# Optimization experiments

Hardware: AMD Instinct MI355X
Metric: run time of the kernel (lower is better)

The kernel has to match this reference:

```python
import jax, jax.numpy as jnp
import numpy as np

NUM_CLASSES = 81
B, P = 32, 32768

def setup_inputs() -> dict:
    key = jax.random.key(0)
    k1, k2, k3, k4, k5 = jax.random.split(key, 5)
    loc_t = jax.random.normal(k1, (B, P, 4), jnp.float32)
    loc_data = jax.random.normal(k2, (B, P, 4), jnp.float32)
    conf_data = jax.random.normal(k3, (B, P, NUM_CLASSES), jnp.float32)
    r = jax.random.uniform(k4, (B, P))
    cls = jax.random.randint(k5, (B, P), 1, NUM_CLASSES)
    conf_t = jnp.where(r < 0.02, cls, jnp.where(r < 0.04, -1, 0)).astype(jnp.int32)
    return {"loc_t": loc_t, "loc_data": loc_data, "conf_t": conf_t, "conf_data": conf_data}

def reference(loc_t, loc_data, conf_t, conf_data):
    num, num_priors, C = conf_data.shape
    pos = conf_t > 0           # [B,P] positive anchors
    regard = conf_t == -1      # [B,P] ignored anchors
    conf_t = jnp.where(regard, 0, conf_t)

    # ---- localization: smooth L1 over positive anchors, summed ----
    diff = jnp.abs(loc_data - loc_t)
    sl1 = jnp.where(diff < 1.0, 0.5 * diff * diff, diff - 0.5)
    loss_l = jnp.sum(sl1 * pos[..., None].astype(sl1.dtype))

    # ---- hard-negative mining score (log_sum_exp with GLOBAL max, as in source) ----
    m = jax.lax.stop_gradient(jnp.max(conf_data))
    lse_global = jnp.log(jnp.sum(jnp.exp(conf_data - m), axis=-1)) + m  # [B,P]
    gathered = jnp.take_along_axis(conf_data, conf_t[..., None], axis=-1)[..., 0]  # [B,P]
    loss_c = lse_global - gathered
    loss_c = jnp.where(pos | regard, 0.0, loss_c)

    # double argsort -> rank of each anchor in descending loss order
    order = jnp.argsort(-loss_c, axis=1)
    rank = jnp.argsort(order, axis=1)
    num_pos = jnp.sum(pos, axis=1, keepdims=True)                     # [B,1]
    num_neg = jnp.minimum(3 * num_pos, num_priors - 1)                # [B,1]
    neg = rank < num_neg                                              # [B,P]

    # ---- classification: cross-entropy over pos|neg anchors, summed ----
    ce = jax.nn.logsumexp(conf_data, axis=-1) - gathered              # [B,P]
    loss_conf = jnp.sum(jnp.where(pos | neg, ce, 0.0))

    N = jnp.sum(num_pos).astype(jnp.float32)
    return (loss_l / N, loss_conf / N)
```

## Files before the change

### kernel.cpp

```cpp
#include <hip/hip_runtime.h>
#include <cstdint>

#define NUM_CLASSES 81
#define BB 32
#define PP 32768
#define CA 64
#define TPB 256
#define CHUNK_FLOATS (CA * NUM_CLASSES)
#define CHUNK_F4 (CHUNK_FLOATS / 4)
#define NCHUNK (BB * PP / CA)
#define GRID_MAIN 768
#define NP_STRIDE 32

__device__ __forceinline__ unsigned f2key(float f) {
    unsigned u = __float_as_uint(f);
    return u ^ (unsigned)(((int)u >> 31) | (int)0x80000000u);
}
__device__ __forceinline__ float key2f(unsigned k) {
    unsigned u = (k & 0x80000000u) ? (k ^ 0x80000000u) : ~k;
    return __uint_as_float(u);
}


__global__ void mbl_zero_kernel(unsigned* __restrict__ p, int n) {
    int i = blockIdx.x * 256 + threadIdx.x;
    if (i < n) p[i] = 0u;
}

__global__ __launch_bounds__(TPB, 4) void mbl_main_kernel(
    const float* __restrict__ loc_t, const float* __restrict__ loc_data,
    const int* __restrict__ conf_t, const float* __restrict__ conf,
    float* __restrict__ loss_c, float* __restrict__ acc, int* __restrict__ num_pos)
{
    __shared__ __align__(16) float tile[2][CHUNK_FLOATS];
    __shared__ float wred[2][TPB / 64];

    const int t = threadIdx.x;
    const int lane = t & 63;
    const int w = t >> 6;
    const int q = lane >> 4;
    const int a_loc = (w << 4) | (lane & 15);

    float sum_ll = 0.f, sum_pce = 0.f;

    int c = blockIdx.x;
    {
        const float4* src = (const float4*)(conf + (size_t)c * CHUNK_FLOATS);
        float4* dst = (float4*)tile[0];
        #pragma unroll
        for (int i = 0; i < 5; ++i) dst[t + i * TPB] = src[t + i * TPB];
        if (t < CHUNK_F4 - 5 * TPB) dst[t + 5 * TPB] = src[t + 5 * TPB];
    }
    int parity = 0;
    const int stride = gridDim.x;
    for (; c < NCHUNK; c += stride) {
        __syncthreads();
        const int nc = c + stride;
        if (nc < NCHUNK) {
            const float4* src = (const float4*)(conf + (size_t)nc * CHUNK_FLOATS);
            float4* dst = (float4*)tile[parity ^ 1];
            #pragma unroll
            for (int i = 0; i < 5; ++i) dst[t + i * TPB] = src[t + i * TPB];
            if (t < CHUNK_F4 - 5 * TPB) dst[t + 5 * TPB] = src[t + 5 * TPB];
        }
        const float* cp = tile[parity] + a_loc * NUM_CLASSES + q * 20;
        float s = 0.f;
        #pragma unroll
        for (int j = 0; j < 20; ++j) s += __expf(cp[j]);
        if (q == 3) s += __expf(cp[20]);
        s += __shfl_xor(s, 16);
        s += __shfl_xor(s, 32);

        bool posl = false;
        if (q == 0) {
            const int idx = c * CA + a_loc;
            const int label = conf_t[idx];
            posl = label > 0;
            const bool regard = label == -1;
            const int lab = label < 0 ? 0 : label;
            const float g = tile[parity][a_loc * NUM_CLASSES + lab];
            const float ce = __logf(s) - g;
            loss_c[idx] = (posl || regard) ? 0.f : ce;
            if (posl) {
                float4 a4 = ((const float4*)loc_data)[idx];
                float4 b4 = ((const float4*)loc_t)[idx];
                float d0 = fabsf(a4.x - b4.x), d1 = fabsf(a4.y - b4.y);
                float d2 = fabsf(a4.z - b4.z), d3 = fabsf(a4.w - b4.w);
                sum_ll += (d0 < 1.f) ? 0.5f * d0 * d0 : d0 - 0.5f;
                sum_ll += (d1 < 1.f) ? 0.5f * d1 * d1 : d1 - 0.5f;
                sum_ll += (d2 < 1.f) ? 0.5f * d2 * d2 : d2 - 0.5f;
                sum_ll += (d3 < 1.f) ? 0.5f * d3 * d3 : d3 - 0.5f;
                sum_pce += ce;
            }
        }
        unsigned long long bal = __ballot(posl);
        if (lane == 0 && bal)
            atomicAdd(&num_pos[(c >> 9) * NP_STRIDE], (int)__popcll(bal));
        parity ^= 1;
    }
    #pragma unroll
    for (int off = 32; off > 0; off >>= 1) {
        sum_ll += __shfl_down(sum_ll, off);
        sum_pce += __shfl_down(sum_pce, off);
    }
    if (lane == 0) { wred[0][w] = sum_ll; wred[1][w] = sum_pce; }
    __syncthreads();
    if (t == 0) {
        float s0 = 0.f, s1 = 0.f;
        #pragma unroll
        for (int i = 0; i < TPB / 64; ++i) { s0 += wred[0][i]; s1 += wred[1][i]; }
        atomicAdd(&acc[0], s0);
        atomicAdd(&acc[1], s1);
    }
}

__global__ __launch_bounds__(256) void mbl_hist_kernel(
    const float* __restrict__ loss_c, const unsigned* __restrict__ prefix,
    unsigned* __restrict__ ghist, int shift, unsigned mask)
{
    const int b = blockIdx.x >> 4;
    const int slice = blockIdx.x & 15;
    const int t = threadIdx.x;
    __shared__ unsigned h[256];
    h[t] = 0u;
    __syncthreads();
    const unsigned pref = prefix[b];
    const float4* r4 = (const float4*)(loss_c + (size_t)b * PP + slice * 2048);
    #pragma unroll
    for (int i = 0; i < 2; ++i) {
        float4 v = r4[t + 256 * i];
        unsigned k0 = f2key(v.x), k1 = f2key(v.y), k2 = f2key(v.z), k3 = f2key(v.w);
        if ((k0 & mask) == pref) atomicAdd(&h[(k0 >> shift) & 255u], 1u);
        if ((k1 & mask) == pref) atomicAdd(&h[(k1 >> shift) & 255u], 1u);
        if ((k2 & mask) == pref) atomicAdd(&h[(k2 >> shift) & 255u], 1u);
        if ((k3 & mask) == pref) atomicAdd(&h[(k3 >> shift) & 255u], 1u);
    }
    __syncthreads();
    unsigned cnt = h[t];
    if (cnt) atomicAdd(&ghist[b * 256 + t], cnt);
}

__global__ __launch_bounds__(256) void mbl_pick_kernel(
    unsigned* __restrict__ ghist, unsigned* __restrict__ prefix,
    unsigned* __restrict__ remaining, const int* __restrict__ num_pos,
    int shift, int first)
{
    const int b = blockIdx.x;
    const int t = threadIdx.x;
    __shared__ unsigned suf[256];
    __shared__ unsigned sh_k;
    if (t == 0) {
        unsigned k;
        if (first) {
            int kk = 3 * num_pos[b * NP_STRIDE];
            if (kk > PP - 1) kk = PP - 1;
            if (kk <= 0) { prefix[b] = 0xFFFFFFFFu; remaining[b] = 0u; k = 0u; }
            else k = (unsigned)kk;
        } else {
            k = remaining[b];
        }
        sh_k = k;
    }
    __syncthreads();
    const unsigned krem = sh_k;
    if (krem == 0u) return;

    unsigned hv = ghist[b * 256 + t];
    ghist[b * 256 + t] = 0u;
    suf[t] = hv;
    __syncthreads();
    #pragma unroll
    for (int step = 1; step < 256; step <<= 1) {
        unsigned v = suf[t] + ((t + step < 256) ? suf[t + step] : 0u);
        __syncthreads();
        suf[t] = v;
        __syncthreads();
    }
    const unsigned above = (t == 255) ? 0u : suf[t + 1];
    if (suf[t] >= krem && above < krem) {
        prefix[b] |= ((unsigned)t) << shift;
        remaining[b] = krem - above;
    }
}

__global__ __launch_bounds__(256) void mbl_sum_kernel(
    const float* __restrict__ loss_c, const unsigned* __restrict__ prefix,
    float* __restrict__ acc)
{
    const int b = blockIdx.x >> 4;
    const int slice = blockIdx.x & 15;
    const int t = threadIdx.x;
    const int lane = t & 63;
    const int w = t >> 6;
    const unsigned T = prefix[b];
    const float4* r4 = (const float4*)(loss_c + (size_t)b * PP + slice * 2048);
    float partial = 0.f;
    #pragma unroll
    for (int i = 0; i < 2; ++i) {
        float4 v = r4[t + 256 * i];
        if (f2key(v.x) > T) partial += v.x;
        if (f2key(v.y) > T) partial += v.y;
        if (f2key(v.z) > T) partial += v.z;
        if (f2key(v.w) > T) partial += v.w;
    }
    #pragma unroll
    for (int off = 32; off > 0; off >>= 1) partial += __shfl_down(partial, off);
    __shared__ float r[4];
    if (lane == 0) r[w] = partial;
    __syncthreads();
    if (t == 0) atomicAdd(&acc[2], r[0] + r[1] + r[2] + r[3]);
}

__global__ void mbl_final_kernel(const float* __restrict__ acc,
                                 const int* __restrict__ num_pos,
                                 const unsigned* __restrict__ prefix,
                                 const unsigned* __restrict__ remaining,
                                 float* __restrict__ out)
{
    if (threadIdx.x == 0 && blockIdx.x == 0) {
        int n = 0;
        float extra = 0.f;
        for (int i = 0; i < BB; ++i) {
            n += num_pos[i * NP_STRIDE];
            unsigned rem = remaining[i];
            if (rem) extra += (float)rem * key2f(prefix[i]);
        }
        const float N = (float)n;
        out[0] = acc[0] / N;
        out[1] = (acc[1] + acc[2] + extra) / N;
    }
}

extern "C" void kernel_launch(void* const* d_in, const int* in_sizes, int n_in,
                              void* d_out, int out_size, void* d_ws, size_t ws_size,
                              hipStream_t stream) {
    const float* loc_t    = (const float*)d_in[0];
    const float* loc_data = (const float*)d_in[1];
    const int*   conf_t   = (const int*)d_in[2];
    const float* conf     = (const float*)d_in[3];
    float* out = (float*)d_out;

    char* ws = (char*)d_ws;
    const size_t off0 = (size_t)BB * PP * sizeof(float);
    float*    loss_c    = (float*)ws;
    float*    acc       = (float*)(ws + off0);
    int*      num_pos   = (int*)(ws + off0 + 256);
    unsigned* prefix    = (unsigned*)(ws + off0 + 4608);
    unsigned* remaining = (unsigned*)(ws + off0 + 4864);
    unsigned* ghist     = (unsigned*)(ws + off0 + 5120);

    mbl_zero_kernel<<<37, 256, 0, stream>>>((unsigned*)(ws + off0), 9472);

    mbl_main_kernel<<<GRID_MAIN, TPB, 0, stream>>>(
        loc_t, loc_data, conf_t, conf, loss_c, acc, num_pos);

    const unsigned masks[4] = {0x00000000u, 0xFF000000u, 0xFFFF0000u, 0xFFFFFF00u};
    for (int p = 0; p < 4; ++p) {
        const int shift = 24 - 8 * p;
        mbl_hist_kernel<<<512, 256, 0, stream>>>(loss_c, prefix, ghist, shift, masks[p]);
        mbl_pick_kernel<<<BB, 256, 0, stream>>>(ghist, prefix, remaining, num_pos,
                                                shift, p == 0 ? 1 : 0);
    }
    mbl_sum_kernel<<<512, 256, 0, stream>>>(loss_c, prefix, acc);
    mbl_final_kernel<<<1, 64, 0, stream>>>(acc, num_pos, prefix, remaining, out);
}
```

Before: 512.9 us.

## Replace multi-pass radix select with single-block-per-batch histogram select; async LDS loads

The main kernel now uses 32-anchor chunks with 8 threads per anchor, a larger grid and higher occupancy bound. It loads conf tiles with global_load_lds direct-to-LDS copies instead of register round-trips. The four hist/pick launch pairs and the separate sum kernel are replaced by one 1024-thread block per batch. That block builds a 4096-bin count and sum histogram, collects the boundary bin into an LDS list, then refines it with two more histogram levels. This removes about ten kernel launches and repeated passes over loss_c. The cost is only 32 blocks doing serial scans, and the boundary list is capped at 16384 entries.

```diff
diff --git a/kernel.cpp b/kernel.cpp
--- a/kernel.cpp
+++ b/kernel.cpp
@@ -4,13 +4,15 @@
 #define NUM_CLASSES 81
 #define BB 32
 #define PP 32768
-#define CA 64
+#define CA 32
 #define TPB 256
 #define CHUNK_FLOATS (CA * NUM_CLASSES)
 #define CHUNK_F4 (CHUNK_FLOATS / 4)
 #define NCHUNK (BB * PP / CA)
-#define GRID_MAIN 768
+#define GRID_MAIN 1792
 #define NP_STRIDE 32
+#define NBIN 4096
+#define LCAP 16384
 
 __device__ __forceinline__ unsigned f2key(float f) {
     unsigned u = __float_as_uint(f);
@@ -21,13 +23,16 @@
     return __uint_as_float(u);
 }
 
+#define GLDS16(gp, lp) __builtin_amdgcn_global_load_lds( \
+    (const __attribute__((address_space(1))) void*)(gp), \
+    (__attribute__((address_space(3))) void*)(lp), 16, 0, 0)
+
 
 __global__ void mbl_zero_kernel(unsigned* __restrict__ p, int n) {
-    int i = blockIdx.x * 256 + threadIdx.x;
-    if (i < n) p[i] = 0u;
-}
-
-__global__ __launch_bounds__(TPB, 4) void mbl_main_kernel(
+    for (int i = threadIdx.x; i < n; i += 1024) p[i] = 0u;
+}
+
+__global__ __launch_bounds__(TPB, 7) void mbl_main_kernel(
     const float* __restrict__ loc_t, const float* __restrict__ loc_data,
     const int* __restrict__ conf_t, const float* __restrict__ conf,
     float* __restrict__ loss_c, float* __restrict__ acc, int* __restrict__ num_pos)
@@ -37,49 +42,50 @@
 
     const int t = threadIdx.x;
     const int lane = t & 63;
-    const int w = t >> 6;
-    const int q = lane >> 4;
-    const int a_loc = (w << 4) | (lane & 15);
+    const int g = t >> 3;
+    const int r = t & 7;
 
     float sum_ll = 0.f, sum_pce = 0.f;
 
     int c = blockIdx.x;
     {
-        const float4* src = (const float4*)(conf + (size_t)c * CHUNK_FLOATS);
-        float4* dst = (float4*)tile[0];
-        #pragma unroll
-        for (int i = 0; i < 5; ++i) dst[t + i * TPB] = src[t + i * TPB];
-        if (t < CHUNK_F4 - 5 * TPB) dst[t + 5 * TPB] = src[t + 5 * TPB];
-    }
+        const float4* s4 = (const float4*)(conf + (size_t)c * CHUNK_FLOATS);
+        float4* d4 = (float4*)tile[0];
+        GLDS16(s4 + t, d4 + t);
+        GLDS16(s4 + t + 256, d4 + t + 256);
+        if (t < CHUNK_F4 - 512) GLDS16(s4 + t + 512, d4 + t + 512);
+    }
+    __syncthreads();
+
     int parity = 0;
     const int stride = gridDim.x;
     for (; c < NCHUNK; c += stride) {
-        __syncthreads();
         const int nc = c + stride;
         if (nc < NCHUNK) {
-            const float4* src = (const float4*)(conf + (size_t)nc * CHUNK_FLOATS);
-            float4* dst = (float4*)tile[parity ^ 1];
-            #pragma unroll
-            for (int i = 0; i < 5; ++i) dst[t + i * TPB] = src[t + i * TPB];
-            if (t < CHUNK_F4 - 5 * TPB) dst[t + 5 * TPB] = src[t + 5 * TPB];
-        }
-        const float* cp = tile[parity] + a_loc * NUM_CLASSES + q * 20;
+            const float4* s4 = (const float4*)(conf + (size_t)nc * CHUNK_FLOATS);
+            float4* d4 = (float4*)tile[parity ^ 1];
+            GLDS16(s4 + t, d4 + t);
+            GLDS16(s4 + t + 256, d4 + t + 256);
+            if (t < CHUNK_F4 - 512) GLDS16(s4 + t + 512, d4 + t + 512);
+        }
+        const float* cp = tile[parity] + g * NUM_CLASSES + r * 10;
         float s = 0.f;
         #pragma unroll
-        for (int j = 0; j < 20; ++j) s += __expf(cp[j]);
-        if (q == 3) s += __expf(cp[20]);
-        s += __shfl_xor(s, 16);
-        s += __shfl_xor(s, 32);
+        for (int j = 0; j < 10; ++j) s += __expf(cp[j]);
+        if (r == 0) s += __expf(tile[parity][g * NUM_CLASSES + 80]);
+        s += __shfl_xor(s, 1);
+        s += __shfl_xor(s, 2);
+        s += __shfl_xor(s, 4);
 
         bool posl = false;
-        if (q == 0) {
-            const int idx = c * CA + a_loc;
+        if (r == 0) {
+            const int idx = c * CA + g;
             const int label = conf_t[idx];
             posl = label > 0;
             const bool regard = label == -1;
             const int lab = label < 0 ? 0 : label;
-            const float g = tile[parity][a_loc * NUM_CLASSES + lab];
-            const float ce = __logf(s) - g;
+            const float gv = tile[parity][g * NUM_CLASSES + lab];
+            const float ce = __logf(s) - gv;
             loss_c[idx] = (posl || regard) ? 0.f : ce;
             if (posl) {
                 float4 a4 = ((const float4*)loc_data)[idx];
@@ -95,7 +101,8 @@
         }
         unsigned long long bal = __ballot(posl);
         if (lane == 0 && bal)
-            atomicAdd(&num_pos[(c >> 9) * NP_STRIDE], (int)__popcll(bal));
+            atomicAdd(&num_pos[(c >> 10) * NP_STRIDE], (int)__popcll(bal));
+        __syncthreads();
         parity ^= 1;
     }
     #pragma unroll
@@ -103,6 +110,7 @@
         sum_ll += __shfl_down(sum_ll, off);
         sum_pce += __shfl_down(sum_pce, off);
     }
+    const int w = t >> 6;
     if (lane == 0) { wred[0][w] = sum_ll; wred[1][w] = sum_pce; }
     __syncthreads();
     if (t == 0) {
@@ -114,120 +122,154 @@
     }
 }
 
-__global__ __launch_bounds__(256) void mbl_hist_kernel(
-    const float* __restrict__ loss_c, const unsigned* __restrict__ prefix,
-    unsigned* __restrict__ ghist, int shift, unsigned mask)
+__global__ __launch_bounds__(1024) void mbl_select_kernel(
+    const float* __restrict__ loss_c, const int* __restrict__ num_pos,
+    float* __restrict__ acc)
 {
-    const int b = blockIdx.x >> 4;
-    const int slice = blockIdx.x & 15;
-    const int t = threadIdx.x;
-    __shared__ unsigned h[256];
-    h[t] = 0u;
-    __syncthreads();
-    const unsigned pref = prefix[b];
-    const float4* r4 = (const float4*)(loss_c + (size_t)b * PP + slice * 2048);
-    #pragma unroll
-    for (int i = 0; i < 2; ++i) {
-        float4 v = r4[t + 256 * i];
-        unsigned k0 = f2key(v.x), k1 = f2key(v.y), k2 = f2key(v.z), k3 = f2key(v.w);
-        if ((k0 & mask) == pref) atomicAdd(&h[(k0 >> shift) & 255u], 1u);
-        if ((k1 & mask) == pref) atomicAdd(&h[(k1 >> shift) & 255u], 1u);
-        if ((k2 & mask) == pref) atomicAdd(&h[(k2 >> shift) & 255u], 1u);
-        if ((k3 & mask) == pref) atomicAdd(&h[(k3 >> shift) & 255u], 1u);
-    }
-    __syncthreads();
-    unsigned cnt = h[t];
-    if (cnt) atomicAdd(&ghist[b * 256 + t], cnt);
-}
-
-__global__ __launch_bounds__(256) void mbl_pick_kernel(
-    unsigned* __restrict__ ghist, unsigned* __restrict__ prefix,
-    unsigned* __restrict__ remaining, const int* __restrict__ num_pos,
-    int shift, int first)
-{
+    __shared__ unsigned cnt[NBIN];
+    __shared__ float fsum[NBIN];
+    __shared__ float list[LCAP];
+    __shared__ unsigned sh_nlist, sh_B, sh_r, sh_D1, sh_r2, sh_D0, sh_rem;
+    __shared__ float sh_above;
+    __shared__ float wr[16];
+
     const int b = blockIdx.x;
     const int t = threadIdx.x;
-    __shared__ unsigned suf[256];
-    __shared__ unsigned sh_k;
+    int k = 3 * num_pos[b * NP_STRIDE];
+    if (k > PP - 1) k = PP - 1;
+    if (k <= 0) return;
+
+    #pragma unroll
+    for (int i = 0; i < NBIN / 1024; ++i) { cnt[t + i * 1024] = 0u; fsum[t + i * 1024] = 0.f; }
+    if (t == 0) sh_nlist = 0u;
+    __syncthreads();
+
+    const float4* r4 = (const float4*)(loss_c + (size_t)b * PP);
+    float4 vv[8];
+    #pragma unroll
+    for (int i = 0; i < 8; ++i) vv[i] = r4[t + i * 1024];
+    #pragma unroll
+    for (int i = 0; i < 8; ++i) {
+        float vals[4] = {vv[i].x, vv[i].y, vv[i].z, vv[i].w};
+        #pragma unroll
+        for (int j = 0; j < 4; ++j) {
+            float v = vals[j];
+            unsigned bin = (f2key(v) >> 19) - 4096u;
+            bin = bin > 4095u ? 4095u : bin;
+            atomicAdd(&cnt[bin], 1u);
+            atomicAdd(&fsum[bin], v);
+        }
+    }
+    __syncthreads();
+
+    for (int step = 1; step < NBIN; step <<= 1) {
+        unsigned c0[4]; float s0[4];
+        #pragma unroll
+        for (int i = 0; i < 4; ++i) {
+            int j = t + i * 1024, jj = j + step;
+            c0[i] = cnt[j] + (jj < NBIN ? cnt[jj] : 0u);
+            s0[i] = fsum[j] + (jj < NBIN ? fsum[jj] : 0.f);
+        }
+        __syncthreads();
+        #pragma unroll
+        for (int i = 0; i < 4; ++i) { int j = t + i * 1024; cnt[j] = c0[i]; fsum[j] = s0[i]; }
+        __syncthreads();
+    }
+    const unsigned kk = (unsigned)k;
+    #pragma unroll
+    for (int i = 0; i < 4; ++i) {
+        int j = t + i * 1024;
+        unsigned here = cnt[j], above = (j < NBIN - 1) ? cnt[j + 1] : 0u;
+        if (here >= kk && above < kk) {
+            sh_B = (unsigned)j; sh_r = kk - above;
+            sh_above = (j < NBIN - 1) ? fsum[j + 1] : 0.f;
+        }
+    }
+    __syncthreads();
+    const unsigned B = sh_B;
+    const unsigned r = sh_r;
+    const float sum_above = sh_above;
+
+    #pragma unroll
+    for (int i = 0; i < 8; ++i) {
+        float vals[4] = {vv[i].x, vv[i].y, vv[i].z, vv[i].w};
+        #pragma unroll
+        for (int j = 0; j < 4; ++j) {
+            float v = vals[j];
+            unsigned bin = (f2key(v) >> 19) - 4096u;
+            bin = bin > 4095u ? 4095u : bin;
+            if (bin == B) { unsigned p = atomicAdd(&sh_nlist, 1u); if (p < LCAP) list[p] = v; }
+        }
+    }
+    __syncthreads();
+    unsigned n = sh_nlist; if (n > LCAP) n = LCAP;
+
+    cnt[t] = 0u;
+    __syncthreads();
+    for (unsigned e = t; e < n; e += 1024)
+        atomicAdd(&cnt[(f2key(list[e]) >> 9) & 1023u], 1u);
+    __syncthreads();
+    for (int step = 1; step < 1024; step <<= 1) {
+        unsigned v = cnt[t] + (t + step < 1024 ? cnt[t + step] : 0u);
+        __syncthreads(); cnt[t] = v; __syncthreads();
+    }
+    {
+        unsigned here = cnt[t], above = (t < 1023) ? cnt[t + 1] : 0u;
+        if (here >= r && above < r) { sh_D1 = (unsigned)t; sh_r2 = r - above; }
+    }
+    __syncthreads();
+    const unsigned D1 = sh_D1;
+    const unsigned r2 = sh_r2;
+
+    if (t < 512) cnt[t] = 0u;
+    __syncthreads();
+    for (unsigned e = t; e < n; e += 1024) {
+        unsigned key = f2key(list[e]);
+        if (((key >> 9) & 1023u) == D1) atomicAdd(&cnt[key & 511u], 1u);
+    }
+    __syncthreads();
+    for (int step = 1; step < 512; step <<= 1) {
+        unsigned v = 0u;
+        if (t < 512) v = cnt[t] + (t + step < 512 ? cnt[t + step] : 0u);
+        __syncthreads();
+        if (t < 512) cnt[t] = v;
+        __syncthreads();
+    }
+    if (t < 512) {
+        unsigned here = cnt[t], above = (t < 511) ? cnt[t + 1] : 0u;
+        if (here >= r2 && above < r2) { sh_D0 = (unsigned)t; sh_rem = r2 - above; }
+    }
+    __syncthreads();
+    const unsigned T = ((B + 4096u) << 19) | (D1 << 9) | sh_D0;
+    const unsigned rem = sh_rem;
+
+    float part = 0.f;
+    for (unsigned e = t; e < n; e += 1024) {
+        float v = list[e];
+        if (f2key(v) > T) part += v;
+    }
+    #pragma unroll
+    for (int off = 32; off > 0; off >>= 1) part += __shfl_down(part, off);
+    if ((t & 63) == 0) wr[t >> 6] = part;
+    __syncthreads();
     if (t == 0) {
-        unsigned k;
-        if (first) {
-            int kk = 3 * num_pos[b * NP_STRIDE];
-            if (kk > PP - 1) kk = PP - 1;
-            if (kk <= 0) { prefix[b] = 0xFFFFFFFFu; remaining[b] = 0u; k = 0u; }
-            else k = (unsigned)kk;
-        } else {
-            k = remaining[b];
-        }
-        sh_k = k;
-    }
-    __syncthreads();
-    const unsigned krem = sh_k;
-    if (krem == 0u) return;
-
-    unsigned hv = ghist[b * 256 + t];
-    ghist[b * 256 + t] = 0u;
-    suf[t] = hv;
-    __syncthreads();
-    #pragma unroll
-    for (int step = 1; step < 256; step <<= 1) {
-        unsigned v = suf[t] + ((t + step < 256) ? suf[t + step] : 0u);
-        __syncthreads();
-        suf[t] = v;
-        __syncthreads();
-    }
-    const unsigned above = (t == 255) ? 0u : suf[t + 1];
-    if (suf[t] >= krem && above < krem) {
-        prefix[b] |= ((unsigned)t) << shift;
-        remaining[b] = krem - above;
-    }
-}
-
-__global__ __launch_bounds__(256) void mbl_sum_kernel(
-    const float* __restrict__ loss_c, const unsigned* __restrict__ prefix,
-    float* __restrict__ acc)
-{
-    const int b = blockIdx.x >> 4;
-    const int slice = blockIdx.x & 15;
-    const int t = threadIdx.x;
-    const int lane = t & 63;
-    const int w = t >> 6;
-    const unsigned T = prefix[b];
-    const float4* r4 = (const float4*)(loss_c + (size_t)b * PP + slice * 2048);
-    float partial = 0.f;
-    #pragma unroll
-    for (int i = 0; i < 2; ++i) {
-        float4 v = r4[t + 256 * i];
-        if (f2key(v.x) > T) partial += v.x;
-        if (f2key(v.y) > T) partial += v.y;
-        if (f2key(v.z) > T) partial += v.z;
-        if (f2key(v.w) > T) partial += v.w;
-    }
-    #pragma unroll
-    for (int off = 32; off > 0; off >>= 1) partial += __shfl_down(partial, off);
-    __shared__ float r[4];
-    if (lane == 0) r[w] = partial;
-    __syncthreads();
-    if (t == 0) atomicAdd(&acc[2], r[0] + r[1] + r[2] + r[3]);
+        float tot = sum_above + (float)rem * key2f(T);
+        #pragma unroll
+        for (int i = 0; i < 16; ++i) tot += wr[i];
+        atomicAdd(&acc[2], tot);
+    }
 }
 
 __global__ void mbl_final_kernel(const float* __restrict__ acc,
                                  const int* __restrict__ num_pos,
-                                 const unsigned* __restrict__ prefix,
-                                 const unsigned* __restrict__ remaining,
                                  float* __restrict__ out)
 {
     if (threadIdx.x == 0 && blockIdx.x == 0) {
         int n = 0;
-        float extra = 0.f;
-        for (int i = 0; i < BB; ++i) {
-            n += num_pos[i * NP_STRIDE];
-            unsigned rem = remaining[i];
-            if (rem) extra += (float)rem * key2f(prefix[i]);
-        }
+        for (int i = 0; i < BB; ++i) n += num_pos[i * NP_STRIDE];
         const float N = (float)n;
         out[0] = acc[0] / N;
-        out[1] = (acc[1] + acc[2] + extra) / N;
+        out[1] = (acc[1] + acc[2]) / N;
     }
 }
 
@@ -242,25 +284,15 @@
 
     char* ws = (char*)d_ws;
     const size_t off0 = (size_t)BB * PP * sizeof(float);
-    float*    loss_c    = (float*)ws;
-    float*    acc       = (float*)(ws + off0);
-    int*      num_pos   = (int*)(ws + off0 + 256);
-    unsigned* prefix    = (unsigned*)(ws + off0 + 4608);
-    unsigned* remaining = (unsigned*)(ws + off0 + 4864);
-    unsigned* ghist     = (unsigned*)(ws + off0 + 5120);
-
-    mbl_zero_kernel<<<37, 256, 0, stream>>>((unsigned*)(ws + off0), 9472);
+    float* loss_c  = (float*)ws;
+    float* acc     = (float*)(ws + off0);
+    int*   num_pos = (int*)(ws + off0 + 256);
+
+    mbl_zero_kernel<<<1, 1024, 0, stream>>>((unsigned*)(ws + off0), 1112);
 
     mbl_main_kernel<<<GRID_MAIN, TPB, 0, stream>>>(
         loc_t, loc_data, conf_t, conf, loss_c, acc, num_pos);
 
-    const unsigned masks[4] = {0x00000000u, 0xFF000000u, 0xFFFF0000u, 0xFFFFFF00u};
-    for (int p = 0; p < 4; ++p) {
-        const int shift = 24 - 8 * p;
-        mbl_hist_kernel<<<512, 256, 0, stream>>>(loss_c, prefix, ghist, shift, masks[p]);
-        mbl_pick_kernel<<<BB, 256, 0, stream>>>(ghist, prefix, remaining, num_pos,
-                                                shift, p == 0 ? 1 : 0);
-    }
-    mbl_sum_kernel<<<512, 256, 0, stream>>>(loss_c, prefix, acc);
-    mbl_final_kernel<<<1, 64, 0, stream>>>(acc, num_pos, prefix, remaining, out);
-}
+    mbl_select_kernel<<<BB, 1024, 0, stream>>>(loss_c, num_pos, acc);
+    mbl_final_kernel<<<1, 64, 0, stream>>>(acc, num_pos, out);
+}
```

After: 559.1 us. 1.09x slower.
